# Optimization experiments

Measured on AMD Instinct MI355X. Metric: run time of the kernel, lower is better.

Reference implementation:

```python
import jax, jax.numpy as jnp
import numpy as np

N_NODES = 100000
N_EDGES = 3200000
D_IN = 128
D_HID = 128
N_CLASSES = 2
N_GRAPHS = 64


def _gcn_conv(x, src, dst, norm, W, b, n_nodes):
    # GCNConv: x' = D^-1/2 (A+I) D^-1/2 (x W) + b  (self-loops already in src/dst)
    h = x @ W                                   # [N, out]
    msg = h[src] * norm[:, None]                # gather + per-edge scale [E', out]
    agg = jax.ops.segment_sum(msg, dst, num_segments=n_nodes)  # scatter-add
    return agg + b


def setup_inputs() -> dict:
    key = jax.random.key(0)
    ks = jax.random.split(key, 10)
    x = jax.random.normal(ks[0], (N_NODES, D_IN), dtype=jnp.float32)
    edge_index = jax.random.randint(ks[1], (2, N_EDGES), 0, N_NODES, dtype=jnp.int32)
    batch = jnp.sort(jax.random.randint(ks[2], (N_NODES,), 0, N_GRAPHS, dtype=jnp.int32))
    s1 = 1.0 / np.sqrt(D_IN)
    s2 = 1.0 / np.sqrt(D_HID)
    W1 = jax.random.uniform(ks[3], (D_IN, D_HID), jnp.float32, -s1, s1)
    b1 = jnp.zeros((D_HID,), jnp.float32)
    W2 = jax.random.uniform(ks[4], (D_HID, D_HID), jnp.float32, -s2, s2)
    b2 = jnp.zeros((D_HID,), jnp.float32)
    Wc = jax.random.uniform(ks[5], (D_HID, N_CLASSES), jnp.float32, -s2, s2)
    bc = jnp.zeros((N_CLASSES,), jnp.float32)
    return {"x": x, "edge_index": edge_index, "batch": batch,
            "W1": W1, "b1": b1, "W2": W2, "b2": b2, "Wc": Wc, "bc": bc,
            "num_graphs": N_GRAPHS}


def reference(x, edge_index, batch, W1, b1, W2, b2, Wc, bc, num_graphs):
    n = x.shape[0]
    loops = jnp.arange(n, dtype=edge_index.dtype)
    src = jnp.concatenate([edge_index[0], loops])
    dst = jnp.concatenate([edge_index[1], loops])
    # symmetric normalization with self-loops (degree over destinations, as PyG)
    deg = jax.ops.segment_sum(jnp.ones_like(dst, dtype=x.dtype), dst, num_segments=n)
    dinv = jnp.where(deg > 0, jax.lax.rsqrt(jnp.maximum(deg, 1.0)), 0.0)
    norm = dinv[src] * dinv[dst]                # [E']

    h = _gcn_conv(x, src, dst, norm, W1, b1, n)
    h = jax.nn.relu(h)                          # dropout is identity at eval
    h = _gcn_conv(h, src, dst, norm, W2, b2, n)

    # global_mean_pool over graph ids
    sums = jax.ops.segment_sum(h, batch, num_segments=num_graphs)      # [G, H]
    cnts = jax.ops.segment_sum(jnp.ones((n,), h.dtype), batch, num_segments=num_graphs)
    pooled = sums / jnp.maximum(cnts, 1.0)[:, None]

    return pooled @ Wc + bc                     # [G, num_classes]
```

## Files before the change

### kernel.cpp

```cpp
#include <hip/hip_runtime.h>
#include <hip/hip_bf16.h>

#define D 128
#define NGRAPH 64
#define POOLBLK 256
#define PBCHUNK 4096
#define WINSZ 256
#define WINSLOTS 16384
#define XP 136

typedef __attribute__((ext_vector_type(4))) float f32x4;
typedef __attribute__((ext_vector_type(8))) short bf16x8;

__device__ __forceinline__ unsigned short f2bf(float f) {
    union { float f; unsigned int i; } u; u.f = f;
    unsigned int r = u.i + 0x7fffu + ((u.i >> 16) & 1u);
    return (unsigned short)(r >> 16);
}
__device__ __forceinline__ float2 bf2_to_f2(unsigned int u) {
    union { unsigned int i; float f; } a, b;
    a.i = u << 16;
    b.i = u & 0xffff0000u;
    return make_float2(a.f, b.f);
}


__global__ __launch_bounds__(256) void k_part(const int* __restrict__ src,
                                              const int* __restrict__ dst,
                                              int* __restrict__ cursor,
                                              unsigned* __restrict__ ebuf,
                                              int E, int nb) {
    __shared__ unsigned spack[PBCHUNK];
    __shared__ unsigned short sbin[PBCHUNK];
    __shared__ unsigned short slrank[PBCHUNK];
    __shared__ int hist[400];
    __shared__ int base[400];
    int tid = threadIdx.x;
    for (int i = tid; i < nb; i += 256) hist[i] = 0;
    __syncthreads();
    int b0 = blockIdx.x * PBCHUNK;
    int cnt = min(PBCHUNK, E - b0);
    for (int j = tid; j < cnt; j += 256) {
        int s = __builtin_nontemporal_load(&src[b0 + j]);
        int d = __builtin_nontemporal_load(&dst[b0 + j]);
        int bin = d >> 8;
        spack[j] = (unsigned)s | ((unsigned)(d & 255) << 17);
        sbin[j] = (unsigned short)bin;
        slrank[j] = (unsigned short)atomicAdd(&hist[bin], 1);
    }
    __syncthreads();
    for (int i = tid; i < nb; i += 256)
        base[i] = hist[i] ? atomicAdd(&cursor[i], hist[i]) : 0;
    __syncthreads();
    for (int j = tid; j < cnt; j += 256) {
        int bin = sbin[j];
        ebuf[(size_t)bin * WINSLOTS + base[bin] + slrank[j]] = spack[j];
    }
}

__global__ __launch_bounds__(256) void k_csrwin(const unsigned* __restrict__ ebuf,
                                                const int* __restrict__ cursor,
                                                int* __restrict__ csr,
                                                int2* __restrict__ offcnt,
                                                float* __restrict__ dinv, int n) {
    __shared__ int hist[WINSZ];
    __shared__ int lscan[WINSZ];
    __shared__ int sexcl[WINSZ];
    int b = blockIdx.x;
    int tid = threadIdx.x;
    hist[tid] = 0;
    __syncthreads();
    int cnt = cursor[b];
    const unsigned* eb = ebuf + (size_t)b * WINSLOTS;
    for (int j = tid; j < cnt; j += 256)
        atomicAdd(&hist[eb[j] >> 17], 1);
    __syncthreads();
    int deg = hist[tid];
    lscan[tid] = deg;
    __syncthreads();
    for (int off = 1; off < 256; off <<= 1) {
        int y = (tid >= off) ? lscan[tid - off] : 0;
        __syncthreads();
        lscan[tid] += y;
        __syncthreads();
    }
    int excl = lscan[tid] - deg;
    int v = b * WINSZ + tid;
    int gbase = b * WINSLOTS;
    if (v < n) {
        offcnt[v] = make_int2(gbase + excl, deg);
        dinv[v] = rsqrtf((float)(deg + 1));
    }
    hist[tid] = 0;
    sexcl[tid] = excl;
    __syncthreads();
    for (int j = tid; j < cnt; j += 256) {
        unsigned p = eb[j];
        int d8 = (int)(p >> 17);
        int lr = atomicAdd(&hist[d8], 1);
        csr[gbase + sexcl[d8] + lr] = (int)(p & 0x1FFFFu);
    }
}


__global__ __launch_bounds__(256) void k_prep(const float* __restrict__ W1,
                                              const float* __restrict__ W2,
                                              const float* __restrict__ Wc,
                                              const float* __restrict__ b2,
                                              const float* __restrict__ bc,
                                              float* __restrict__ Weff,
                                              float* __restrict__ beff,
                                              unsigned short* __restrict__ W1bfT) {
    int t = threadIdx.x;
    int i = t >> 1, c = t & 1;
    float acc = 0.f;
    for (int k = 0; k < D; ++k) acc += W2[i * D + k] * Wc[k * 2 + c];
    Weff[i * 2 + c] = acc;
    if (i == 0) {
        float s = 0.f;
        for (int k = 0; k < D; ++k) s += b2[k] * Wc[k * 2 + c];
        beff[c] = s + bc[c];
    }
    for (int e = t; e < D * D; e += 256) {
        int n = e >> 7, k = e & 127;
        W1bfT[n * D + k] = f2bf(W1[k * D + n]);
    }
}


__global__ __launch_bounds__(256) void k_gemm_mfma(const float* __restrict__ X,
                                                   const unsigned short* __restrict__ W1bfT,
                                                   unsigned short* __restrict__ H, int nrows) {
    __shared__ unsigned short xs[64][XP];
    __shared__ unsigned short wt[128][XP];
    int tid = threadIdx.x;
    int m0 = blockIdx.x * 64;
    {
        const uint4* wsrc = (const uint4*)W1bfT;
        for (int i = tid; i < 2048; i += 256) {
            uint4 v = wsrc[i];
            int elt = i * 8;
            int r = elt >> 7, c = elt & 127;
            *(uint4*)&wt[r][c] = v;
        }
    }
    {
        for (int i = tid; i < 2048; i += 256) {
            int elt = i * 4;
            int r = elt >> 7, c = elt & 127;
            int gr = m0 + r;
            float4 v = (gr < nrows) ? *(const float4*)&X[(size_t)gr * D + c]
                                    : make_float4(0.f, 0.f, 0.f, 0.f);
            ushort4 bv;
            bv.x = f2bf(v.x); bv.y = f2bf(v.y); bv.z = f2bf(v.z); bv.w = f2bf(v.w);
            *(ushort4*)&xs[r][c] = bv;
        }
    }
    __syncthreads();
    int wv = tid >> 6, lane = tid & 63;
    int lrow = lane & 15, lk = (lane >> 4) * 8;
    f32x4 acc[8];
#pragma unroll
    for (int i = 0; i < 8; ++i) acc[i] = (f32x4){0.f, 0.f, 0.f, 0.f};
#pragma unroll
    for (int kk = 0; kk < 128; kk += 32) {
        bf16x8 a = *(bf16x8*)&xs[wv * 16 + lrow][kk + lk];
#pragma unroll
        for (int nt = 0; nt < 8; ++nt) {
            bf16x8 b = *(bf16x8*)&wt[nt * 16 + lrow][kk + lk];
            acc[nt] = __builtin_amdgcn_mfma_f32_16x16x32_bf16(a, b, acc[nt], 0, 0, 0);
        }
    }
    int orow = m0 + wv * 16 + (lane >> 4) * 4;
#pragma unroll
    for (int nt = 0; nt < 8; ++nt) {
#pragma unroll
        for (int r = 0; r < 4; ++r) {
            int gr = orow + r;
            if (gr < nrows) H[(size_t)gr * D + nt * 16 + lrow] = f2bf(acc[nt][r]);
        }
    }
}


__global__ __launch_bounds__(256) void k_agg_proj(const unsigned short* __restrict__ H,
                                                  const int2* __restrict__ offcnt,
                                                  const int* __restrict__ csr,
                                                  const float* __restrict__ dinv,
                                                  const float* __restrict__ bias,
                                                  const float* __restrict__ Weff,
                                                  float2* __restrict__ z, int n) {
    int wid = threadIdx.x >> 6;
    int lane = threadIdx.x & 63;
    int v = blockIdx.x * 4 + wid;
    if (v >= n) return;
    float dv = dinv[v];
    int l2 = lane * 2;
    unsigned us = *(const unsigned*)(H + (size_t)v * D + l2);
    float2 hs = bf2_to_f2(us);
    float dv2 = dv * dv;
    float2 acc = make_float2(hs.x * dv2, hs.y * dv2);
    int2 oc = offcnt[v];
    int e = oc.x, eE = oc.x + oc.y;
    for (; e + 3 < eE; e += 4) {
        int s0 = csr[e], s1 = csr[e + 1], s2 = csr[e + 2], s3 = csr[e + 3];
        unsigned u0 = *(const unsigned*)(H + (size_t)s0 * D + l2);
        unsigned u1 = *(const unsigned*)(H + (size_t)s1 * D + l2);
        unsigned u2 = *(const unsigned*)(H + (size_t)s2 * D + l2);
        unsigned u3 = *(const unsigned*)(H + (size_t)s3 * D + l2);
        float w0 = dinv[s0] * dv, w1 = dinv[s1] * dv;
        float w2 = dinv[s2] * dv, w3 = dinv[s3] * dv;
        float2 h0 = bf2_to_f2(u0), h1 = bf2_to_f2(u1);
        float2 h2 = bf2_to_f2(u2), h3 = bf2_to_f2(u3);
        acc.x += h0.x * w0; acc.y += h0.y * w0;
        acc.x += h1.x * w1; acc.y += h1.y * w1;
        acc.x += h2.x * w2; acc.y += h2.y * w2;
        acc.x += h3.x * w3; acc.y += h3.y * w3;
    }
    for (; e < eE; ++e) {
        int s0 = csr[e];
        float w0 = dinv[s0] * dv;
        unsigned u0 = *(const unsigned*)(H + (size_t)s0 * D + l2);
        float2 h0 = bf2_to_f2(u0);
        acc.x += h0.x * w0; acc.y += h0.y * w0;
    }
    float2 b = ((const float2*)bias)[lane];
    acc.x = fmaxf(acc.x + b.x, 0.f);
    acc.y = fmaxf(acc.y + b.y, 0.f);
    float4 wv = *(const float4*)&Weff[l2 * 2];
    float z0 = acc.x * wv.x + acc.y * wv.z;
    float z1 = acc.x * wv.y + acc.y * wv.w;
#pragma unroll
    for (int off = 32; off >= 1; off >>= 1) {
        z0 += __shfl_xor(z0, off, 64);
        z1 += __shfl_xor(z1, off, 64);
    }
    if (lane == 0) z[v] = make_float2(z0, z1);
}


__global__ __launch_bounds__(256) void k_pool_edges(const float2* __restrict__ z,
                                                    const int* __restrict__ src,
                                                    const int* __restrict__ dst,
                                                    const float* __restrict__ dinv,
                                                    const int* __restrict__ batch,
                                                    float* __restrict__ tsum,
                                                    int* __restrict__ cnt,
                                                    int n, int E) {
    __shared__ float t[NGRAPH * 2];
    __shared__ int scnt[NGRAPH];
    int tid = threadIdx.x;
    if (tid < NGRAPH * 2) t[tid] = 0.f;
    if (tid < NGRAPH) scnt[tid] = 0;
    __syncthreads();

    int i = (blockIdx.x * 256 + tid) * 4;
    int stride = POOLBLK * 256 * 4;
    for (; i < E; i += stride) {
        if (i + 3 < E) {
            int4 s4 = *(const int4*)&src[i];
            int4 d4 = *(const int4*)&dst[i];
            float w0 = dinv[s4.x] * dinv[d4.x];
            float w1 = dinv[s4.y] * dinv[d4.y];
            float w2 = dinv[s4.z] * dinv[d4.z];
            float w3 = dinv[s4.w] * dinv[d4.w];
            float2 z0 = z[s4.x], z1 = z[s4.y], z2 = z[s4.z], z3 = z[s4.w];
            int g0 = batch[d4.x], g1 = batch[d4.y], g2 = batch[d4.z], g3 = batch[d4.w];
            atomicAdd(&t[g0 * 2],     w0 * z0.x);
            atomicAdd(&t[g0 * 2 + 1], w0 * z0.y);
            atomicAdd(&t[g1 * 2],     w1 * z1.x);
            atomicAdd(&t[g1 * 2 + 1], w1 * z1.y);
            atomicAdd(&t[g2 * 2],     w2 * z2.x);
            atomicAdd(&t[g2 * 2 + 1], w2 * z2.y);
            atomicAdd(&t[g3 * 2],     w3 * z3.x);
            atomicAdd(&t[g3 * 2 + 1], w3 * z3.y);
        } else {
            for (int j = i; j < E; ++j) {
                int s = src[j], d = dst[j];
                float w = dinv[s] * dinv[d];
                float2 zv = z[s];
                int g = batch[d];
                atomicAdd(&t[g * 2],     w * zv.x);
                atomicAdd(&t[g * 2 + 1], w * zv.y);
            }
        }
    }
    for (int v = blockIdx.x * 256 + tid; v < n; v += POOLBLK * 256) {
        float dv = dinv[v];
        float2 zv = z[v];
        int g = batch[v];
        float w = dv * dv;
        atomicAdd(&t[g * 2],     w * zv.x);
        atomicAdd(&t[g * 2 + 1], w * zv.y);
        atomicAdd(&scnt[g], 1);
    }
    __syncthreads();
    if (tid < NGRAPH * 2 && t[tid] != 0.f) atomicAdd(&tsum[tid], t[tid]);
    if (tid < NGRAPH && scnt[tid]) atomicAdd(&cnt[tid], scnt[tid]);
}

__global__ void k_classify(const float* __restrict__ tsum, const int* __restrict__ cnt,
                           const float* __restrict__ beff, const float* __restrict__ bc,
                           float* __restrict__ out) {
    int t = threadIdx.x;
    if (t >= NGRAPH * 2) return;
    int g = t >> 1, c = t & 1;
    int cg = cnt[g];
    out[t] = cg ? (tsum[t] / (float)cg + beff[c]) : bc[c];
}


extern "C" void kernel_launch(void* const* d_in, const int* in_sizes, int n_in,
                              void* d_out, int out_size, void* d_ws, size_t ws_size,
                              hipStream_t stream) {
    const float* x    = (const float*)d_in[0];
    const int*   ei   = (const int*)d_in[1];
    const int*   batch= (const int*)d_in[2];
    const float* W1   = (const float*)d_in[3];
    const float* b1   = (const float*)d_in[4];
    const float* W2   = (const float*)d_in[5];
    const float* b2   = (const float*)d_in[6];
    const float* Wc   = (const float*)d_in[7];
    const float* bc   = (const float*)d_in[8];

    const int n = in_sizes[0] / D;
    const int E = in_sizes[1] / 2;
    const int* src = ei;
    const int* dst = ei + E;
    const int nb = (n + WINSZ - 1) / WINSZ;

    char* ws = (char*)d_ws;
    size_t off = 0;
    auto carve = [&](size_t bytes) -> char* {
        char* p = ws + off;
        off = (off + bytes + 255) & ~(size_t)255;
        return p;
    };
    unsigned short* bufBF = (unsigned short*)carve((size_t)n * D * 2);
    float2* z     = (float2*)carve((size_t)n * 8);
    unsigned* ebuf= (unsigned*)carve((size_t)nb * WINSLOTS * 4);
    int*   csr    = (int*)  carve((size_t)nb * WINSLOTS * 4);
    int*   cursor = (int*)  carve((512 + NGRAPH * 2 + NGRAPH) * 4);
    float* tsum   = (float*)(cursor + 512);
    int*   cnt    = (int*)  (tsum + NGRAPH * 2);
    int2*  offcnt = (int2*) carve((size_t)n * 8);
    float* dinv   = (float*)carve((size_t)n * 4);
    float* Weff   = (float*)carve(D * 2 * 4);
    float* beff   = (float*)carve(2 * 4);
    unsigned short* W1bfT = (unsigned short*)carve(D * D * 2);

    hipMemsetAsync(cursor, 0, (512 + NGRAPH * 2 + NGRAPH) * 4, stream);

    k_part<<<(E + PBCHUNK - 1) / PBCHUNK, 256, 0, stream>>>(src, dst, cursor, ebuf, E, nb);
    k_csrwin<<<nb, 256, 0, stream>>>(ebuf, cursor, csr, offcnt, dinv, n);
    k_prep<<<1, 256, 0, stream>>>(W1, W2, Wc, b2, bc, Weff, beff, W1bfT);

    k_gemm_mfma<<<(n + 63) / 64, 256, 0, stream>>>(x, W1bfT, bufBF, n);
    k_agg_proj<<<(n + 3) / 4, 256, 0, stream>>>(bufBF, offcnt, csr, dinv, b1, Weff, z, n);

    k_pool_edges<<<POOLBLK, 256, 0, stream>>>(z, src, dst, dinv, batch, tsum, cnt, n, E);
    k_classify<<<1, 128, 0, stream>>>(tsum, cnt, beff, bc, (float*)d_out);
}
```

Before: 305.9 us.

## Fold memset into prep kernel, fuse W1 transpose into GEMM, unroll gather, per-wave pool bins

The memset is replaced by zeroing inside k_prep, which now runs first, saving one launch. W1 is now transposed and converted to bf16 inside every GEMM block instead of in a separate prep pass, which removes a dependency but repeats that conversion work per block with strided LDS writes. The aggregation loop gains an 8-wide unrolled stage so more gathers are in flight, and the pool kernel uses per-wave shared bins to cut LDS atomic contention. Together these touch several unrelated stages.

```diff
diff --git a/kernel.cpp b/kernel.cpp
--- a/kernel.cpp
+++ b/kernel.cpp
@@ -22,6 +22,28 @@
     a.i = u << 16;
     b.i = u & 0xffff0000u;
     return make_float2(a.f, b.f);
+}
+
+
+__global__ __launch_bounds__(256) void k_prep(const float* __restrict__ W2,
+                                              const float* __restrict__ Wc,
+                                              const float* __restrict__ b2,
+                                              const float* __restrict__ bc,
+                                              float* __restrict__ Weff,
+                                              float* __restrict__ beff,
+                                              int* __restrict__ zero_region,
+                                              int zero_words) {
+    int t = threadIdx.x;
+    int i = t >> 1, c = t & 1;
+    float acc = 0.f;
+    for (int k = 0; k < D; ++k) acc += W2[i * D + k] * Wc[k * 2 + c];
+    Weff[i * 2 + c] = acc;
+    if (i == 0) {
+        float s = 0.f;
+        for (int k = 0; k < D; ++k) s += b2[k] * Wc[k * 2 + c];
+        beff[c] = s + bc[c];
+    }
+    for (int j = t; j < zero_words; j += 256) zero_region[j] = 0;
 }
 
 
@@ -103,58 +125,32 @@
 }
 
 
-__global__ __launch_bounds__(256) void k_prep(const float* __restrict__ W1,
-                                              const float* __restrict__ W2,
-                                              const float* __restrict__ Wc,
-                                              const float* __restrict__ b2,
-                                              const float* __restrict__ bc,
-                                              float* __restrict__ Weff,
-                                              float* __restrict__ beff,
-                                              unsigned short* __restrict__ W1bfT) {
-    int t = threadIdx.x;
-    int i = t >> 1, c = t & 1;
-    float acc = 0.f;
-    for (int k = 0; k < D; ++k) acc += W2[i * D + k] * Wc[k * 2 + c];
-    Weff[i * 2 + c] = acc;
-    if (i == 0) {
-        float s = 0.f;
-        for (int k = 0; k < D; ++k) s += b2[k] * Wc[k * 2 + c];
-        beff[c] = s + bc[c];
-    }
-    for (int e = t; e < D * D; e += 256) {
-        int n = e >> 7, k = e & 127;
-        W1bfT[n * D + k] = f2bf(W1[k * D + n]);
-    }
-}
-
-
 __global__ __launch_bounds__(256) void k_gemm_mfma(const float* __restrict__ X,
-                                                   const unsigned short* __restrict__ W1bfT,
+                                                   const float* __restrict__ W1,
                                                    unsigned short* __restrict__ H, int nrows) {
     __shared__ unsigned short xs[64][XP];
     __shared__ unsigned short wt[128][XP];
     int tid = threadIdx.x;
     int m0 = blockIdx.x * 64;
-    {
-        const uint4* wsrc = (const uint4*)W1bfT;
-        for (int i = tid; i < 2048; i += 256) {
-            uint4 v = wsrc[i];
-            int elt = i * 8;
-            int r = elt >> 7, c = elt & 127;
-            *(uint4*)&wt[r][c] = v;
-        }
-    }
-    {
-        for (int i = tid; i < 2048; i += 256) {
-            int elt = i * 4;
-            int r = elt >> 7, c = elt & 127;
-            int gr = m0 + r;
-            float4 v = (gr < nrows) ? *(const float4*)&X[(size_t)gr * D + c]
-                                    : make_float4(0.f, 0.f, 0.f, 0.f);
-            ushort4 bv;
-            bv.x = f2bf(v.x); bv.y = f2bf(v.y); bv.z = f2bf(v.z); bv.w = f2bf(v.w);
-            *(ushort4*)&xs[r][c] = bv;
-        }
+    for (int i = tid; i < 2048; i += 256) {
+        int elt = i * 8;
+        int k = elt >> 7, n0 = elt & 127;
+        float4 a = *(const float4*)&W1[k * D + n0];
+        float4 b = *(const float4*)&W1[k * D + n0 + 4];
+        wt[n0 + 0][k] = f2bf(a.x); wt[n0 + 1][k] = f2bf(a.y);
+        wt[n0 + 2][k] = f2bf(a.z); wt[n0 + 3][k] = f2bf(a.w);
+        wt[n0 + 4][k] = f2bf(b.x); wt[n0 + 5][k] = f2bf(b.y);
+        wt[n0 + 6][k] = f2bf(b.z); wt[n0 + 7][k] = f2bf(b.w);
+    }
+    for (int i = tid; i < 2048; i += 256) {
+        int elt = i * 4;
+        int r = elt >> 7, c = elt & 127;
+        int gr = m0 + r;
+        float4 v = (gr < nrows) ? *(const float4*)&X[(size_t)gr * D + c]
+                                : make_float4(0.f, 0.f, 0.f, 0.f);
+        ushort4 bv;
+        bv.x = f2bf(v.x); bv.y = f2bf(v.y); bv.z = f2bf(v.z); bv.w = f2bf(v.w);
+        *(ushort4*)&xs[r][c] = bv;
     }
     __syncthreads();
     int wv = tid >> 6, lane = tid & 63;
@@ -202,6 +198,22 @@
     float2 acc = make_float2(hs.x * dv2, hs.y * dv2);
     int2 oc = offcnt[v];
     int e = oc.x, eE = oc.x + oc.y;
+    for (; e + 7 < eE; e += 8) {
+        int s[8];
+#pragma unroll
+        for (int j = 0; j < 8; ++j) s[j] = csr[e + j];
+        unsigned u[8];
+#pragma unroll
+        for (int j = 0; j < 8; ++j) u[j] = *(const unsigned*)(H + (size_t)s[j] * D + l2);
+        float w[8];
+#pragma unroll
+        for (int j = 0; j < 8; ++j) w[j] = dinv[s[j]] * dv;
+#pragma unroll
+        for (int j = 0; j < 8; ++j) {
+            float2 h = bf2_to_f2(u[j]);
+            acc.x += h.x * w[j]; acc.y += h.y * w[j];
+        }
+    }
     for (; e + 3 < eE; e += 4) {
         int s0 = csr[e], s1 = csr[e + 1], s2 = csr[e + 2], s3 = csr[e + 3];
         unsigned u0 = *(const unsigned*)(H + (size_t)s0 * D + l2);
@@ -247,11 +259,12 @@
                                                     float* __restrict__ tsum,
                                                     int* __restrict__ cnt,
                                                     int n, int E) {
-    __shared__ float t[NGRAPH * 2];
-    __shared__ int scnt[NGRAPH];
+    __shared__ float t[4][NGRAPH * 2];
+    __shared__ int scnt[4][NGRAPH];
     int tid = threadIdx.x;
-    if (tid < NGRAPH * 2) t[tid] = 0.f;
-    if (tid < NGRAPH) scnt[tid] = 0;
+    int wv = tid >> 6;
+    for (int j = tid; j < 4 * NGRAPH * 2; j += 256) ((float*)t)[j] = 0.f;
+    for (int j = tid; j < 4 * NGRAPH; j += 256) ((int*)scnt)[j] = 0;
     __syncthreads();
 
     int i = (blockIdx.x * 256 + tid) * 4;
@@ -266,22 +279,22 @@
             float w3 = dinv[s4.w] * dinv[d4.w];
             float2 z0 = z[s4.x], z1 = z[s4.y], z2 = z[s4.z], z3 = z[s4.w];
             int g0 = batch[d4.x], g1 = batch[d4.y], g2 = batch[d4.z], g3 = batch[d4.w];
-            atomicAdd(&t[g0 * 2],     w0 * z0.x);
-            atomicAdd(&t[g0 * 2 + 1], w0 * z0.y);
-            atomicAdd(&t[g1 * 2],     w1 * z1.x);
-            atomicAdd(&t[g1 * 2 + 1], w1 * z1.y);
-            atomicAdd(&t[g2 * 2],     w2 * z2.x);
-            atomicAdd(&t[g2 * 2 + 1], w2 * z2.y);
-            atomicAdd(&t[g3 * 2],     w3 * z3.x);
-            atomicAdd(&t[g3 * 2 + 1], w3 * z3.y);
+            atomicAdd(&t[wv][g0 * 2],     w0 * z0.x);
+            atomicAdd(&t[wv][g0 * 2 + 1], w0 * z0.y);
+            atomicAdd(&t[wv][g1 * 2],     w1 * z1.x);
+            atomicAdd(&t[wv][g1 * 2 + 1], w1 * z1.y);
+            atomicAdd(&t[wv][g2 * 2],     w2 * z2.x);
+            atomicAdd(&t[wv][g2 * 2 + 1], w2 * z2.y);
+            atomicAdd(&t[wv][g3 * 2],     w3 * z3.x);
+            atomicAdd(&t[wv][g3 * 2 + 1], w3 * z3.y);
         } else {
             for (int j = i; j < E; ++j) {
                 int s = src[j], d = dst[j];
                 float w = dinv[s] * dinv[d];
                 float2 zv = z[s];
                 int g = batch[d];
-                atomicAdd(&t[g * 2],     w * zv.x);
-                atomicAdd(&t[g * 2 + 1], w * zv.y);
+                atomicAdd(&t[wv][g * 2],     w * zv.x);
+                atomicAdd(&t[wv][g * 2 + 1], w * zv.y);
             }
         }
     }
@@ -290,13 +303,19 @@
         float2 zv = z[v];
         int g = batch[v];
         float w = dv * dv;
-        atomicAdd(&t[g * 2],     w * zv.x);
-        atomicAdd(&t[g * 2 + 1], w * zv.y);
-        atomicAdd(&scnt[g], 1);
-    }
-    __syncthreads();
-    if (tid < NGRAPH * 2 && t[tid] != 0.f) atomicAdd(&tsum[tid], t[tid]);
-    if (tid < NGRAPH && scnt[tid]) atomicAdd(&cnt[tid], scnt[tid]);
+        atomicAdd(&t[wv][g * 2],     w * zv.x);
+        atomicAdd(&t[wv][g * 2 + 1], w * zv.y);
+        atomicAdd(&scnt[wv][g], 1);
+    }
+    __syncthreads();
+    if (tid < NGRAPH * 2) {
+        float s = t[0][tid] + t[1][tid] + t[2][tid] + t[3][tid];
+        if (s != 0.f) atomicAdd(&tsum[tid], s);
+    }
+    if (tid < NGRAPH) {
+        int s = scnt[0][tid] + scnt[1][tid] + scnt[2][tid] + scnt[3][tid];
+        if (s) atomicAdd(&cnt[tid], s);
+    }
 }
 
 __global__ void k_classify(const float* __restrict__ tsum, const int* __restrict__ cnt,
@@ -340,22 +359,20 @@
     float2* z     = (float2*)carve((size_t)n * 8);
     unsigned* ebuf= (unsigned*)carve((size_t)nb * WINSLOTS * 4);
     int*   csr    = (int*)  carve((size_t)nb * WINSLOTS * 4);
-    int*   cursor = (int*)  carve((512 + NGRAPH * 2 + NGRAPH) * 4);
+    const int zero_words = 512 + NGRAPH * 2 + NGRAPH;
+    int*   cursor = (int*)  carve(zero_words * 4);
     float* tsum   = (float*)(cursor + 512);
     int*   cnt    = (int*)  (tsum + NGRAPH * 2);
     int2*  offcnt = (int2*) carve((size_t)n * 8);
     float* dinv   = (float*)carve((size_t)n * 4);
     float* Weff   = (float*)carve(D * 2 * 4);
     float* beff   = (float*)carve(2 * 4);
-    unsigned short* W1bfT = (unsigned short*)carve(D * D * 2);
-
-    hipMemsetAsync(cursor, 0, (512 + NGRAPH * 2 + NGRAPH) * 4, stream);
-
+
+    k_prep<<<1, 256, 0, stream>>>(W2, Wc, b2, bc, Weff, beff, cursor, zero_words);
     k_part<<<(E + PBCHUNK - 1) / PBCHUNK, 256, 0, stream>>>(src, dst, cursor, ebuf, E, nb);
     k_csrwin<<<nb, 256, 0, stream>>>(ebuf, cursor, csr, offcnt, dinv, n);
-    k_prep<<<1, 256, 0, stream>>>(W1, W2, Wc, b2, bc, Weff, beff, W1bfT);
-
-    k_gemm_mfma<<<(n + 63) / 64, 256, 0, stream>>>(x, W1bfT, bufBF, n);
+
+    k_gemm_mfma<<<(n + 63) / 64, 256, 0, stream>>>(x, W1, bufBF, n);
     k_agg_proj<<<(n + 3) / 4, 256, 0, stream>>>(bufBF, offcnt, csr, dinv, b1, Weff, z, n);
 
     k_pool_edges<<<POOLBLK, 256, 0, stream>>>(z, src, dst, dinv, batch, tsum, cnt, n, E);
```

After: 290.1 us. -5.2%, faster.
